# Performance work log

Measured on AMD Instinct MI355X. Metric: run time of the kernel, lower is better.

Reference implementation:

```python
import jax, jax.numpy as jnp
import numpy as np

B, S, D = 2, 2048, 1024
H = 16
HD = D // H  # head_dim = 64
NEG = -1e30  # finite stand-in for -inf; masked entries are zeroed after softmax so math matches


def setup_inputs() -> dict:
    key = jax.random.key(0)
    ks = jax.random.split(key, 10)
    q = jax.random.normal(ks[0], (B, S, D), dtype=jnp.float32)
    k = jax.random.normal(ks[1], (B, S, D), dtype=jnp.float32)
    v = jax.random.normal(ks[2], (B, S, D), dtype=jnp.float32)
    mask = jax.random.randint(ks[3], (B, S), 0, 2).astype(bool)
    s = 1.0 / np.sqrt(D)
    Wq = jax.random.uniform(ks[4], (D, D), jnp.float32, -s, s)
    bq = jax.random.uniform(ks[5], (D,), jnp.float32, -s, s)
    Wk = jax.random.uniform(ks[6], (D, D), jnp.float32, -s, s)
    bk = jax.random.uniform(ks[7], (D,), jnp.float32, -s, s)
    Wv = jax.random.uniform(ks[8], (D, D), jnp.float32, -s, s)
    bv = jax.random.uniform(ks[9], (D,), jnp.float32, -s, s)
    return {"q": q, "k": k, "v": v, "mask": mask,
            "Wq": Wq, "bq": bq, "Wk": Wk, "bk": bk, "Wv": Wv, "bv": bv}


def _split_heads(x):
    # [B,S,D] -> [H,B,S,HD]  (matches permute(2,0,1,3) in torch)
    return x.reshape(B, S, H, HD).transpose(2, 0, 1, 3)


def reference(q, k, v, mask, Wq, bq, Wk, bk, Wv, bv):
    mq = _split_heads(q @ Wq.T + bq)
    mk = _split_heads(k @ Wk.T + bk)
    mv = _split_heads(v @ Wv.T + bv)
    # scores: [H,B,Sq,Sk]
    scores = jnp.einsum('hbqd,hbkd->hbqk', mq, mk) / jnp.sqrt(jnp.float32(HD))
    pair_mask = (mask[:, :, None] & mask[:, None, :])[None]  # [1,B,S,S]
    scores = jnp.where(pair_mask, scores, NEG)
    attn = jax.nn.softmax(scores, axis=-1)
    attn = jnp.where(pair_mask, attn, 0.0)
    out = jnp.einsum('hbqk,hbkd->hbqd', attn, mv)
    # [H,B,S,HD] -> [B,S,D]
    return out.transpose(1, 2, 0, 3).reshape(B, S, H * HD)
```

## Files before the change

### kernel.cpp

```cpp
#include <hip/hip_runtime.h>
#include <math.h>

#define B_ 2
#define S_ 2048
#define D_ 1024
#define H_ 16
#define HD_ 64
#define LOG2E 1.44269504088896340736f

typedef __bf16 bf16_t;
typedef bf16_t bf16x8 __attribute__((ext_vector_type(8)));
typedef bf16_t bf16x4v __attribute__((ext_vector_type(4)));
typedef float f32x4 __attribute__((ext_vector_type(4)));

#define GLOBAL_LOAD_LDS16(gp, lp)                                              \
    __builtin_amdgcn_global_load_lds(                                          \
        (const __attribute__((address_space(1))) void*)(gp),                   \
        (__attribute__((address_space(3))) void*)(lp), 16, 0, 0)

static __device__ __forceinline__ float exp2_raw(float x)
{
    float r;
    asm("v_exp_f32 %0, %1" : "=v"(r) : "v"(x));
    return r;
}

__global__ __launch_bounds__(256) void cvt_kernel(
    const float* __restrict__ wq, const float* __restrict__ wk,
    const float* __restrict__ wv,
    bf16_t* __restrict__ wqb, bf16_t* __restrict__ wkb, bf16_t* __restrict__ wvb)
{
    const size_t NW = (size_t)1 << 18;
    size_t g = (size_t)blockIdx.x * 256 + threadIdx.x;
    if (g >= 3 * NW) return;

    int t = (int)(g >> 18);
    size_t off = (g & (NW - 1)) * 4;
    const float* src = (t == 0) ? wq : (t == 1) ? wk : wv;
    bf16_t* dst      = (t == 0) ? wqb : (t == 1) ? wkb : wvb;

    float4 f = *(const float4*)(src + off);
    bf16x4v o;
    o[0] = (bf16_t)f.x; o[1] = (bf16_t)f.y;
    o[2] = (bf16_t)f.z; o[3] = (bf16_t)f.w;
    *(bf16x4v*)(dst + off) = o;
}

__global__ __launch_bounds__(256) void proj_mfma(
    const float* __restrict__ X0, const float* __restrict__ X1,
    const float* __restrict__ X2, const bf16_t* __restrict__ W0,
    const bf16_t* __restrict__ W1, const bf16_t* __restrict__ W2,
    const float* __restrict__ b0, const float* __restrict__ b1,
    const float* __restrict__ b2, bf16_t* __restrict__ o0,
    bf16_t* __restrict__ o1, bf16_t* __restrict__ o2)
{
    __shared__ __align__(16) bf16_t As[2][128 * 32];
    __shared__ __align__(16) bf16_t Bs[2][128 * 32];

    const int z = blockIdx.z;
    const float*  X = (z == 0) ? X0 : (z == 1) ? X1 : X2;
    const bf16_t* W = (z == 0) ? W0 : (z == 1) ? W1 : W2;
    const float* bias = (z == 0) ? b0 : (z == 1) ? b1 : b2;
    bf16_t* out = (z == 0) ? o0 : (z == 1) ? o1 : o2;
    const float oscale = (z == 0) ? (0.125f * LOG2E) : 1.0f;

    const int tid  = threadIdx.x;
    const int w    = tid >> 6;
    const int lane = tid & 63;
    const int L    = lane & 15;
    const int quad = lane >> 4;
    const int wr   = (w >> 1) * 64;
    const int wc   = (w & 1) * 64;
    const int row0 = blockIdx.x * 128;
    const int col0 = blockIdx.y * 128;

    const int lr = lane >> 2;
    const int lc = (lane & 3) * 8;
    const int arow = tid >> 3;
    const int ac4  = (tid & 7) * 4;

    f32x4 acc[4][4];
    #pragma unroll
    for (int i = 0; i < 4; ++i)
        #pragma unroll
        for (int j = 0; j < 4; ++j) {
            acc[i][j][0] = 0.f; acc[i][j][1] = 0.f;
            acc[i][j][2] = 0.f; acc[i][j][3] = 0.f;
        }

    float4 ax[4];
    const float* xbase = X + (size_t)(row0 + arow) * D_ + ac4;

    #pragma unroll
    for (int rr = 0; rr < 4; ++rr)
        ax[rr] = *(const float4*)(xbase + (size_t)rr * 32 * D_);
    #pragma unroll
    for (int rr = 0; rr < 4; ++rr) {
        bf16x4v t4;
        t4[0] = (bf16_t)ax[rr].x; t4[1] = (bf16_t)ax[rr].y;
        t4[2] = (bf16_t)ax[rr].z; t4[3] = (bf16_t)ax[rr].w;
        *(bf16x4v*)&As[0][(arow + rr * 32) * 32 + ac4] = t4;
    }
    #pragma unroll
    for (int i = 0; i < 2; ++i) {
        const int rA = i * 64 + w * 16;
        GLOBAL_LOAD_LDS16(W + (size_t)(col0 + rA + lr) * D_ + lc, &Bs[0][rA * 32]);
    }
    #pragma unroll
    for (int rr = 0; rr < 4; ++rr)
        ax[rr] = *(const float4*)(xbase + (size_t)rr * 32 * D_ + 32);
    __syncthreads();

    for (int kk = 0; kk < 32; ++kk) {
        const int cur = kk & 1;

        if (kk < 31) {
            #pragma unroll
            for (int rr = 0; rr < 4; ++rr) {
                bf16x4v t4;
                t4[0] = (bf16_t)ax[rr].x; t4[1] = (bf16_t)ax[rr].y;
                t4[2] = (bf16_t)ax[rr].z; t4[3] = (bf16_t)ax[rr].w;
                *(bf16x4v*)&As[cur ^ 1][(arow + rr * 32) * 32 + ac4] = t4;
            }
            const int k1 = (kk + 1) * 32;
            #pragma unroll
            for (int i = 0; i < 2; ++i) {
                const int rA = i * 64 + w * 16;
                GLOBAL_LOAD_LDS16(W + (size_t)(col0 + rA + lr) * D_ + k1 + lc,
                                  &Bs[cur ^ 1][rA * 32]);
            }
        }
        if (kk < 30) {
            const int k2 = (kk + 2) * 32;
            #pragma unroll
            for (int rr = 0; rr < 4; ++rr)
                ax[rr] = *(const float4*)(xbase + (size_t)rr * 32 * D_ + k2);
        }

        bf16x8 aF[4], bF[4];
        #pragma unroll
        for (int t = 0; t < 4; ++t) {
            aF[t] = *(const bf16x8*)&As[cur][(wr + t * 16 + L) * 32 + quad * 8];
            bF[t] = *(const bf16x8*)&Bs[cur][(wc + t * 16 + L) * 32 + quad * 8];
        }
        #pragma unroll
        for (int mt = 0; mt < 4; ++mt)
            #pragma unroll
            for (int nt = 0; nt < 4; ++nt)
                acc[mt][nt] = __builtin_amdgcn_mfma_f32_16x16x32_bf16(
                    aF[mt], bF[nt], acc[mt][nt], 0, 0, 0);

        __syncthreads();
    }

    if (z == 2) {
        #pragma unroll
        for (int nt = 0; nt < 4; ++nt) {
            const int j  = col0 + wc + nt * 16 + L;
            const float bval = bias[j];
            const int h  = j >> 6;
            const int hd = j & 63;
            #pragma unroll
            for (int mt = 0; mt < 4; ++mt) {
                const int n0 = row0 + wr + mt * 16 + quad * 4;
                const int b  = n0 >> 11;
                const int s  = n0 & (S_ - 1);
                bf16x4v p;
                #pragma unroll
                for (int r = 0; r < 4; ++r)
                    p[r] = (bf16_t)(acc[mt][nt][r] + bval);
                *(bf16x4v*)(out + ((size_t)(b * H_ + h) * HD_ + hd) * S_ + s) = p;
            }
        }
    } else {
        #pragma unroll
        for (int nt = 0; nt < 4; ++nt) {
            const int j  = col0 + wc + nt * 16 + L;
            const float bval = bias[j];
            const int h  = j >> 6;
            const int hd = j & 63;
            #pragma unroll
            for (int mt = 0; mt < 4; ++mt)
                #pragma unroll
                for (int r = 0; r < 4; ++r) {
                    const int n = row0 + wr + mt * 16 + quad * 4 + r;
                    const int b = n >> 11;
                    const int s = n & (S_ - 1);
                    out[((((size_t)b * H_ + h) * S_ + s) * HD_) + hd] =
                        (bf16_t)((acc[mt][nt][r] + bval) * oscale);
                }
        }
    }
}

__global__ __launch_bounds__(256) void attn_kernel(
    const bf16_t* __restrict__ Q, const bf16_t* __restrict__ K,
    const bf16_t* __restrict__ Vt, const int* __restrict__ mask,
    float* __restrict__ out)
{
    __shared__ bf16_t Ks[2][64 * 64];
    __shared__ bf16_t Vs[2][64 * 64];
    __shared__ bf16_t Pt[4][32 * 64];

    const int tid  = threadIdx.x;
    const int w    = tid >> 6;
    const int lane = tid & 63;
    const int L    = lane & 15;
    const int quad = lane >> 4;
    const int L7   = L & 7;

    const float VB = -8.0f * LOG2E;
    const float MB = -1.44269504e30f;

    const int orig = blockIdx.x + 16 * (blockIdx.y + 16 * blockIdx.z);
    const int work = (orig & 7) * 64 + (orig >> 3);
    const int q0   = (work & 15) * 128;
    const int h    = (work >> 4) & 15;
    const int b    = work >> 8;
    const int bh   = b * H_ + h;

    const bf16_t* kbase = K  + (size_t)bh * S_ * HD_;
    const bf16_t* vbase = Vt + (size_t)bh * HD_ * S_;
    const int*    mrow  = mask + b * S_;

    const int sr  = tid >> 3;
    const int c8  = tid & 7;
    const int sc2 = c8 * 8;
    const int swz = ((c8 ^ (sr & 7)) * 8);
    const int st0 = sr * 64 + swz;
    const int st1 = (sr + 32) * 64 + swz;

    bf16x8 aQ[2][2];
    #pragma unroll
    for (int qb = 0; qb < 2; ++qb) {
        const bf16_t* qp = Q + ((size_t)bh * S_ + q0 + w * 32 + qb * 16 + L) * HD_;
        aQ[qb][0] = *(const bf16x8*)(qp + quad * 8);
        aQ[qb][1] = *(const bf16x8*)(qp + 32 + quad * 8);
    }

    f32x4 o[2][4];
    #pragma unroll
    for (int qb = 0; qb < 2; ++qb)
        #pragma unroll
        for (int f = 0; f < 4; ++f) {
            o[qb][f][0]=0.f; o[qb][f][1]=0.f; o[qb][f][2]=0.f; o[qb][f][3]=0.f;
        }
    f32x4 ol[2];
    #pragma unroll
    for (int qb = 0; qb < 2; ++qb) {
        ol[qb][0]=0.f; ol[qb][1]=0.f; ol[qb][2]=0.f; ol[qb][3]=0.f;
    }

    bf16x8 ones;
    #pragma unroll
    for (int i = 0; i < 8; ++i) ones[i] = (bf16_t)1.0f;

    bf16x8 kr0, kr1, vr0, vr1;
    f32x4  bias_c[4], bias_n[4];
    kr0 = *(const bf16x8*)(kbase + (size_t)sr * HD_ + sc2);
    kr1 = *(const bf16x8*)(kbase + (size_t)(sr + 32) * HD_ + sc2);
    vr0 = *(const bf16x8*)(vbase + (size_t)sr * S_ + sc2);
    vr1 = *(const bf16x8*)(vbase + (size_t)(sr + 32) * S_ + sc2);
    #pragma unroll
    for (int f = 0; f < 4; ++f) {
        int4 mi = *(const int4*)(mrow + f * 16 + quad * 4);
        bias_c[f][0] = mi.x ? VB : MB;
        bias_c[f][1] = mi.y ? VB : MB;
        bias_c[f][2] = mi.z ? VB : MB;
        bias_c[f][3] = mi.w ? VB : MB;
    }

    *(bf16x8*)&Ks[0][st0] = kr0;
    *(bf16x8*)&Ks[0][st1] = kr1;
    *(bf16x8*)&Vs[0][st0] = vr0;
    *(bf16x8*)&Vs[0][st1] = vr1;

    kr0 = *(const bf16x8*)(kbase + (size_t)(64 + sr) * HD_ + sc2);
    kr1 = *(const bf16x8*)(kbase + (size_t)(64 + sr + 32) * HD_ + sc2);
    vr0 = *(const bf16x8*)(vbase + (size_t)sr * S_ + 64 + sc2);
    vr1 = *(const bf16x8*)(vbase + (size_t)(sr + 32) * S_ + 64 + sc2);
    #pragma unroll
    for (int f = 0; f < 4; ++f) {
        int4 mi = *(const int4*)(mrow + 64 + f * 16 + quad * 4);
        bias_n[f][0] = mi.x ? VB : MB;
        bias_n[f][1] = mi.y ? VB : MB;
        bias_n[f][2] = mi.z ? VB : MB;
        bias_n[f][3] = mi.w ? VB : MB;
    }

    __syncthreads();

    for (int t = 0; t < 32; ++t) {
        const int cur = t & 1;
        bf16_t* ks  = &Ks[cur][0];
        bf16_t* vs  = &Vs[cur][0];

        if (t < 31) {
            bf16_t* ksn = &Ks[cur ^ 1][0];
            bf16_t* vsn = &Vs[cur ^ 1][0];
            *(bf16x8*)&ksn[st0] = kr0;
            *(bf16x8*)&ksn[st1] = kr1;
            *(bf16x8*)&vsn[st0] = vr0;
            *(bf16x8*)&vsn[st1] = vr1;
        }
        if (t < 30) {
            const int kn = (t + 2) * 64;
            kr0 = *(const bf16x8*)(kbase + (size_t)(kn + sr) * HD_ + sc2);
            kr1 = *(const bf16x8*)(kbase + (size_t)(kn + sr + 32) * HD_ + sc2);
            vr0 = *(const bf16x8*)(vbase + (size_t)sr * S_ + kn + sc2);
            vr1 = *(const bf16x8*)(vbase + (size_t)(sr + 32) * S_ + kn + sc2);
        }

        bf16x8 aK[4][2];
        #pragma unroll
        for (int f = 0; f < 4; ++f) {
            const int row = (f * 16 + L) * 64;
            aK[f][0] = *(const bf16x8*)&ks[row + ((quad ^ L7) * 8)];
            aK[f][1] = *(const bf16x8*)&ks[row + (((4 | quad) ^ L7) * 8)];
        }

        bf16_t* pw = &Pt[w][0];
        #pragma unroll
        for (int qb = 0; qb < 2; ++qb) {
            const int prow = (qb * 16 + L) * 64;
            #pragma unroll
            for (int f = 0; f < 4; ++f) {
                f32x4 z = bias_c[f];
                z = __builtin_amdgcn_mfma_f32_16x16x32_bf16(aK[f][0], aQ[qb][0], z, 0, 0, 0);
                z = __builtin_amdgcn_mfma_f32_16x16x32_bf16(aK[f][1], aQ[qb][1], z, 0, 0, 0);
                bf16x4v p4;
                p4[0] = (bf16_t)exp2_raw(z[0]);
                p4[1] = (bf16_t)exp2_raw(z[1]);
                p4[2] = (bf16_t)exp2_raw(z[2]);
                p4[3] = (bf16_t)exp2_raw(z[3]);
                *(bf16x4v*)&pw[prow + (((f * 2 + (quad >> 1)) ^ L7) * 8) + (quad & 1) * 4] = p4;
            }
        }

        #pragma unroll
        for (int f = 0; f < 4; ++f) bias_c[f] = bias_n[f];
        if (t < 30) {
            const int kn = (t + 2) * 64;
            #pragma unroll
            for (int f = 0; f < 4; ++f) {
                int4 mi = *(const int4*)(mrow + kn + f * 16 + quad * 4);
                bias_n[f][0] = mi.x ? VB : MB;
                bias_n[f][1] = mi.y ? VB : MB;
                bias_n[f][2] = mi.z ? VB : MB;
                bias_n[f][3] = mi.w ? VB : MB;
            }
        }

        bf16x8 aP[2][2];
        #pragma unroll
        for (int qb = 0; qb < 2; ++qb) {
            const int prow = (qb * 16 + L) * 64;
            aP[qb][0] = *(const bf16x8*)&pw[prow + ((quad ^ L7) * 8)];
            aP[qb][1] = *(const bf16x8*)&pw[prow + (((4 | quad) ^ L7) * 8)];
            ol[qb] = __builtin_amdgcn_mfma_f32_16x16x32_bf16(aP[qb][0], ones, ol[qb], 0, 0, 0);
            ol[qb] = __builtin_amdgcn_mfma_f32_16x16x32_bf16(aP[qb][1], ones, ol[qb], 0, 0, 0);
        }

        #pragma unroll
        for (int f = 0; f < 4; ++f) {
            const int row = (f * 16 + L) * 64;
            bf16x8 bV0 = *(const bf16x8*)&vs[row + ((quad ^ L7) * 8)];
            bf16x8 bV1 = *(const bf16x8*)&vs[row + (((4 | quad) ^ L7) * 8)];
            #pragma unroll
            for (int qb = 0; qb < 2; ++qb) {
                o[qb][f] = __builtin_amdgcn_mfma_f32_16x16x32_bf16(aP[qb][0], bV0, o[qb][f], 0, 0, 0);
                o[qb][f] = __builtin_amdgcn_mfma_f32_16x16x32_bf16(aP[qb][1], bV1, o[qb][f], 0, 0, 0);
            }
        }

        __syncthreads();
    }

    #pragma unroll
    for (int qb = 0; qb < 2; ++qb) {
        const int4 m4 = *(const int4*)&mrow[q0 + w * 32 + qb * 16 + quad * 4];
        float inv[4];
        inv[0] = (m4.x && ol[qb][0] > 0.f) ? (1.0f / ol[qb][0]) : 0.0f;
        inv[1] = (m4.y && ol[qb][1] > 0.f) ? (1.0f / ol[qb][1]) : 0.0f;
        inv[2] = (m4.z && ol[qb][2] > 0.f) ? (1.0f / ol[qb][2]) : 0.0f;
        inv[3] = (m4.w && ol[qb][3] > 0.f) ? (1.0f / ol[qb][3]) : 0.0f;

        float* obase = out + ((size_t)b * S_ + q0 + w * 32 + qb * 16 + quad * 4) * D_ + h * HD_;
        #pragma unroll
        for (int f = 0; f < 4; ++f)
            #pragma unroll
            for (int r = 0; r < 4; ++r)
                obase[r * D_ + f * 16 + L] = o[qb][f][r] * inv[r];
    }
}

extern "C" void kernel_launch(void* const* d_in, const int* in_sizes, int n_in,
                              void* d_out, int out_size, void* d_ws, size_t ws_size,
                              hipStream_t stream)
{
    const float* q    = (const float*)d_in[0];
    const float* k    = (const float*)d_in[1];
    const float* v    = (const float*)d_in[2];
    const int*   mask = (const int*)d_in[3];
    const float* Wq   = (const float*)d_in[4];
    const float* bq   = (const float*)d_in[5];
    const float* Wk   = (const float*)d_in[6];
    const float* bk   = (const float*)d_in[7];
    const float* Wv   = (const float*)d_in[8];
    const float* bv   = (const float*)d_in[9];
    float* out = (float*)d_out;

    const size_t PE = (size_t)B_ * S_ * D_;
    const size_t WE = (size_t)D_ * D_;

    bf16_t* wqb = (bf16_t*)d_ws;
    bf16_t* wkb = wqb + WE;
    bf16_t* wvb = wkb + WE;
    bf16_t* mq  = wvb + WE;
    bf16_t* mk  = mq + PE;
    bf16_t* vt  = mk + PE;

    dim3 cgrid(3 * (WE / 4) / 256);
    cvt_kernel<<<cgrid, 256, 0, stream>>>(Wq, Wk, Wv, wqb, wkb, wvb);

    dim3 pgrid(4096 / 128, 1024 / 128, 3);
    proj_mfma<<<pgrid, 256, 0, stream>>>(q, k, v, wqb, wkb, wvb,
                                         bq, bk, bv, mq, mk, vt);

    dim3 agrid(S_ / 128, H_, B_);
    attn_kernel<<<agrid, 256, 0, stream>>>(mq, mk, vt, mask, out);
}
```

Baseline: 239.2 us.

## Pre-convert activations to bf16 and load both GEMM operands via direct-to-LDS

The q/k/v activations are now converted to bf16 in the conversion pre-pass together with the weights. The projection GEMM then loads both operands with global_load_lds into single-buffered shared memory, with two barriers per k-step, replacing the register-staged fp32 loads and double buffering. This simplifies the inner loop and halves activation bytes read by the GEMM. In exchange it adds an extra full read and write of the activations in the pre-pass and gives up the software prefetch overlap.

```diff
diff --git a/kernel.cpp b/kernel.cpp
--- a/kernel.cpp
+++ b/kernel.cpp
@@ -26,18 +26,32 @@
 }
 
 __global__ __launch_bounds__(256) void cvt_kernel(
-    const float* __restrict__ wq, const float* __restrict__ wk,
-    const float* __restrict__ wv,
+    const float* __restrict__ q, const float* __restrict__ k,
+    const float* __restrict__ v, const float* __restrict__ wq,
+    const float* __restrict__ wk, const float* __restrict__ wv,
+    bf16_t* __restrict__ qb, bf16_t* __restrict__ kb, bf16_t* __restrict__ vb,
     bf16_t* __restrict__ wqb, bf16_t* __restrict__ wkb, bf16_t* __restrict__ wvb)
 {
+    const size_t NT = (size_t)1 << 20;
     const size_t NW = (size_t)1 << 18;
     size_t g = (size_t)blockIdx.x * 256 + threadIdx.x;
-    if (g >= 3 * NW) return;
-
-    int t = (int)(g >> 18);
-    size_t off = (g & (NW - 1)) * 4;
-    const float* src = (t == 0) ? wq : (t == 1) ? wk : wv;
-    bf16_t* dst      = (t == 0) ? wqb : (t == 1) ? wkb : wvb;
+
+    const float* src;
+    bf16_t* dst;
+    size_t off;
+    if (g < 3 * NT) {
+        int t = (int)(g >> 20);
+        off = (g & (NT - 1)) * 4;
+        src = (t == 0) ? q : (t == 1) ? k : v;
+        dst = (t == 0) ? qb : (t == 1) ? kb : vb;
+    } else {
+        size_t gw = g - 3 * NT;
+        if (gw >= 3 * NW) return;
+        int t = (int)(gw >> 18);
+        off = (gw & (NW - 1)) * 4;
+        src = (t == 0) ? wq : (t == 1) ? wk : wv;
+        dst = (t == 0) ? wqb : (t == 1) ? wkb : wvb;
+    }
 
     float4 f = *(const float4*)(src + off);
     bf16x4v o;
@@ -47,18 +61,18 @@
 }
 
 __global__ __launch_bounds__(256) void proj_mfma(
-    const float* __restrict__ X0, const float* __restrict__ X1,
-    const float* __restrict__ X2, const bf16_t* __restrict__ W0,
+    const bf16_t* __restrict__ X0, const bf16_t* __restrict__ X1,
+    const bf16_t* __restrict__ X2, const bf16_t* __restrict__ W0,
     const bf16_t* __restrict__ W1, const bf16_t* __restrict__ W2,
     const float* __restrict__ b0, const float* __restrict__ b1,
     const float* __restrict__ b2, bf16_t* __restrict__ o0,
     bf16_t* __restrict__ o1, bf16_t* __restrict__ o2)
 {
-    __shared__ __align__(16) bf16_t As[2][128 * 32];
-    __shared__ __align__(16) bf16_t Bs[2][128 * 32];
+    __shared__ __align__(16) bf16_t As[128 * 32];
+    __shared__ __align__(16) bf16_t Bs[128 * 32];
 
     const int z = blockIdx.z;
-    const float*  X = (z == 0) ? X0 : (z == 1) ? X1 : X2;
+    const bf16_t* X = (z == 0) ? X0 : (z == 1) ? X1 : X2;
     const bf16_t* W = (z == 0) ? W0 : (z == 1) ? W1 : W2;
     const float* bias = (z == 0) ? b0 : (z == 1) ? b1 : b2;
     bf16_t* out = (z == 0) ? o0 : (z == 1) ? o1 : o2;
@@ -76,8 +90,6 @@
 
     const int lr = lane >> 2;
     const int lc = (lane & 3) * 8;
-    const int arow = tid >> 3;
-    const int ac4  = (tid & 7) * 4;
 
     f32x4 acc[4][4];
     #pragma unroll
@@ -88,60 +100,23 @@
             acc[i][j][2] = 0.f; acc[i][j][3] = 0.f;
         }
 
-    float4 ax[4];
-    const float* xbase = X + (size_t)(row0 + arow) * D_ + ac4;
-
-    #pragma unroll
-    for (int rr = 0; rr < 4; ++rr)
-        ax[rr] = *(const float4*)(xbase + (size_t)rr * 32 * D_);
-    #pragma unroll
-    for (int rr = 0; rr < 4; ++rr) {
-        bf16x4v t4;
-        t4[0] = (bf16_t)ax[rr].x; t4[1] = (bf16_t)ax[rr].y;
-        t4[2] = (bf16_t)ax[rr].z; t4[3] = (bf16_t)ax[rr].w;
-        *(bf16x4v*)&As[0][(arow + rr * 32) * 32 + ac4] = t4;
-    }
-    #pragma unroll
-    for (int i = 0; i < 2; ++i) {
-        const int rA = i * 64 + w * 16;
-        GLOBAL_LOAD_LDS16(W + (size_t)(col0 + rA + lr) * D_ + lc, &Bs[0][rA * 32]);
-    }
-    #pragma unroll
-    for (int rr = 0; rr < 4; ++rr)
-        ax[rr] = *(const float4*)(xbase + (size_t)rr * 32 * D_ + 32);
-    __syncthreads();
-
-    for (int kk = 0; kk < 32; ++kk) {
-        const int cur = kk & 1;
-
-        if (kk < 31) {
-            #pragma unroll
-            for (int rr = 0; rr < 4; ++rr) {
-                bf16x4v t4;
-                t4[0] = (bf16_t)ax[rr].x; t4[1] = (bf16_t)ax[rr].y;
-                t4[2] = (bf16_t)ax[rr].z; t4[3] = (bf16_t)ax[rr].w;
-                *(bf16x4v*)&As[cur ^ 1][(arow + rr * 32) * 32 + ac4] = t4;
-            }
-            const int k1 = (kk + 1) * 32;
-            #pragma unroll
-            for (int i = 0; i < 2; ++i) {
-                const int rA = i * 64 + w * 16;
-                GLOBAL_LOAD_LDS16(W + (size_t)(col0 + rA + lr) * D_ + k1 + lc,
-                                  &Bs[cur ^ 1][rA * 32]);
-            }
-        }
-        if (kk < 30) {
-            const int k2 = (kk + 2) * 32;
-            #pragma unroll
-            for (int rr = 0; rr < 4; ++rr)
-                ax[rr] = *(const float4*)(xbase + (size_t)rr * 32 * D_ + k2);
-        }
+    for (int k0 = 0; k0 < D_; k0 += 32) {
+        __syncthreads();
+        #pragma unroll
+        for (int i = 0; i < 2; ++i) {
+            const int rA = i * 64 + w * 16;
+            GLOBAL_LOAD_LDS16(X + (size_t)(row0 + rA + lr) * D_ + k0 + lc,
+                              &As[rA * 32]);
+            GLOBAL_LOAD_LDS16(W + (size_t)(col0 + rA + lr) * D_ + k0 + lc,
+                              &Bs[rA * 32]);
+        }
+        __syncthreads();
 
         bf16x8 aF[4], bF[4];
         #pragma unroll
         for (int t = 0; t < 4; ++t) {
-            aF[t] = *(const bf16x8*)&As[cur][(wr + t * 16 + L) * 32 + quad * 8];
-            bF[t] = *(const bf16x8*)&Bs[cur][(wc + t * 16 + L) * 32 + quad * 8];
+            aF[t] = *(const bf16x8*)&As[(wr + t * 16 + L) * 32 + quad * 8];
+            bF[t] = *(const bf16x8*)&Bs[(wc + t * 16 + L) * 32 + quad * 8];
         }
         #pragma unroll
         for (int mt = 0; mt < 4; ++mt)
@@ -149,8 +124,6 @@
             for (int nt = 0; nt < 4; ++nt)
                 acc[mt][nt] = __builtin_amdgcn_mfma_f32_16x16x32_bf16(
                     aF[mt], bF[nt], acc[mt][nt], 0, 0, 0);
-
-        __syncthreads();
     }
 
     if (z == 2) {
@@ -413,18 +386,23 @@
     const size_t PE = (size_t)B_ * S_ * D_;
     const size_t WE = (size_t)D_ * D_;
 
-    bf16_t* wqb = (bf16_t*)d_ws;
+    bf16_t* qb  = (bf16_t*)d_ws;
+    bf16_t* kb  = qb + PE;
+    bf16_t* vb  = kb + PE;
+    bf16_t* wqb = vb + PE;
     bf16_t* wkb = wqb + WE;
     bf16_t* wvb = wkb + WE;
     bf16_t* mq  = wvb + WE;
     bf16_t* mk  = mq + PE;
     bf16_t* vt  = mk + PE;
 
-    dim3 cgrid(3 * (WE / 4) / 256);
-    cvt_kernel<<<cgrid, 256, 0, stream>>>(Wq, Wk, Wv, wqb, wkb, wvb);
+    const size_t ngroups = 3 * (PE / 4) + 3 * (WE / 4);
+    dim3 cgrid((ngroups + 255) / 256);
+    cvt_kernel<<<cgrid, 256, 0, stream>>>(q, k, v, Wq, Wk, Wv,
+                                          qb, kb, vb, wqb, wkb, wvb);
 
     dim3 pgrid(4096 / 128, 1024 / 128, 3);
-    proj_mfma<<<pgrid, 256, 0, stream>>>(q, k, v, wqb, wkb, wvb,
+    proj_mfma<<<pgrid, 256, 0, stream>>>(qb, kb, vb, wqb, wkb, wvb,
                                          bq, bk, bv, mq, mk, vt);
 
     dim3 agrid(S_ / 128, H_, B_);
```

Result: faster. 218.2 us (-8.8%).
